# Optimization experiments

Hardware: AMD Instinct MI355X
Metric: run time of the kernel (lower is better)

Reference implementation:

```python
import jax, jax.numpy as jnp
import numpy as np

N_TYPES = 4
N_REL = 8
N_HEADS = 8
IN_DIM = 256
N_HID = 128
D_K = N_HID // N_HEADS
N_LAYERS = 2
N_NODES = 100000
N_EDGES = 400000


def setup_inputs() -> dict:
    key = jax.random.key(0)
    ks = jax.random.split(key, 24)
    s = 0.05
    inp = {
        'node_feature': jax.random.normal(ks[0], (N_NODES, IN_DIM), jnp.float32),
        'node_type': jax.random.randint(ks[1], (N_NODES,), 0, N_TYPES),
        'edge_index': jax.random.randint(ks[2], (2, N_EDGES), 0, N_NODES),
        'edge_type': jax.random.randint(ks[3], (N_EDGES,), 0, N_REL),
        # per-type input adapters
        'adapt_w': jax.random.normal(ks[4], (N_TYPES, IN_DIM, N_HID), jnp.float32) * s,
        'adapt_b': jnp.zeros((N_TYPES, N_HID), jnp.float32),
        # HGT conv params, stacked over layers
        'k_w': jax.random.normal(ks[5], (N_LAYERS, N_TYPES, N_HID, N_HID), jnp.float32) * s,
        'k_b': jnp.zeros((N_LAYERS, N_TYPES, N_HID), jnp.float32),
        'q_w': jax.random.normal(ks[6], (N_LAYERS, N_TYPES, N_HID, N_HID), jnp.float32) * s,
        'q_b': jnp.zeros((N_LAYERS, N_TYPES, N_HID), jnp.float32),
        'v_w': jax.random.normal(ks[7], (N_LAYERS, N_TYPES, N_HID, N_HID), jnp.float32) * s,
        'v_b': jnp.zeros((N_LAYERS, N_TYPES, N_HID), jnp.float32),
        'a_w': jax.random.normal(ks[8], (N_LAYERS, N_TYPES, N_HID, N_HID), jnp.float32) * s,
        'a_b': jnp.zeros((N_LAYERS, N_TYPES, N_HID), jnp.float32),
        'rel_pri': jnp.ones((N_LAYERS, N_REL, N_HEADS), jnp.float32),
        'rel_att': jnp.tile(jnp.eye(D_K, dtype=jnp.float32), (N_LAYERS, N_REL, N_HEADS, 1, 1))
                   + jax.random.normal(ks[9], (N_LAYERS, N_REL, N_HEADS, D_K, D_K), jnp.float32) * s,
        'rel_msg': jnp.tile(jnp.eye(D_K, dtype=jnp.float32), (N_LAYERS, N_REL, N_HEADS, 1, 1))
                   + jax.random.normal(ks[10], (N_LAYERS, N_REL, N_HEADS, D_K, D_K), jnp.float32) * s,
        'skip': jnp.ones((N_LAYERS, N_TYPES), jnp.float32),
    }
    return inp


def _per_type_linear(x, w, b, node_type, n_idx):
    # x: [N, din], w: [T, din, dout], b: [T, dout] -> gather row for each node's type
    h_all = jnp.einsum('ni,tio->tno', x, w) + b[:, None, :]  # [T, N, dout]
    return h_all[node_type, n_idx]  # [N, dout]


def _edge_softmax(score, tgt, n):
    # score: [E, H]; softmax over incoming edges of each target node
    m = jax.ops.segment_max(score, tgt, num_segments=n)  # [N, H]
    e = jnp.exp(score - m[tgt])
    z = jax.ops.segment_sum(e, tgt, num_segments=n)
    return e / (z[tgt] + 1e-9)


def _hgt_layer(x, node_type, src, tgt, edge_type,
               kw, kb, qw, qb, vw, vb, aw, ab, pri, att_m, msg_m, skip):
    n = x.shape[0]
    n_idx = jnp.arange(n)
    k = _per_type_linear(x, kw, kb, node_type, n_idx).reshape(n, N_HEADS, D_K)
    q = _per_type_linear(x, qw, qb, node_type, n_idx).reshape(n, N_HEADS, D_K)
    v = _per_type_linear(x, vw, vb, node_type, n_idx).reshape(n, N_HEADS, D_K)
    k_src, v_src, q_tgt = k[src], v[src], q[tgt]  # [E, H, dk]
    # per-relation attention/message transforms, accumulated over small fixed R
    k_rel = jnp.zeros_like(k_src)
    v_rel = jnp.zeros_like(v_src)
    for r in range(N_REL):
        msk = (edge_type == r)[:, None, None]
        k_rel = k_rel + jnp.einsum('ehd,hdf->ehf', jnp.where(msk, k_src, 0.0), att_m[r])
        v_rel = v_rel + jnp.einsum('ehd,hdf->ehf', jnp.where(msk, v_src, 0.0), msg_m[r])
    score = (q_tgt * k_rel).sum(-1) * pri[edge_type] * (1.0 / (D_K ** 0.5))  # [E, H]
    att = _edge_softmax(score, tgt, n)
    agg = jax.ops.segment_sum(att[..., None] * v_rel, tgt, num_segments=n)  # [N, H, dk]
    agg = agg.reshape(n, N_HID)
    trans = _per_type_linear(jax.nn.gelu(agg), aw, ab, node_type, n_idx)
    alpha = jax.nn.sigmoid(skip)[node_type][:, None]
    return trans * alpha + x * (1.0 - alpha)


def reference(node_feature, node_type, edge_index, edge_type,
              adapt_w, adapt_b, k_w, k_b, q_w, q_b, v_w, v_b,
              a_w, a_b, rel_pri, rel_att, rel_msg, skip):
    n = node_feature.shape[0]
    n_idx = jnp.arange(n)
    # per-node-type adapter + tanh (gather-linear-scatter, fully vectorized)
    h = jnp.tanh(_per_type_linear(node_feature, adapt_w, adapt_b, node_type, n_idx))
    src, tgt = edge_index[0], edge_index[1]
    for l in range(N_LAYERS):
        h = _hgt_layer(h, node_type, src, tgt, edge_type,
                       k_w[l], k_b[l], q_w[l], q_b[l], v_w[l], v_b[l],
                       a_w[l], a_b[l], rel_pri[l], rel_att[l], rel_msg[l], skip[l])
    return h
```

## Files before the change

### kernel.cpp

```cpp
#include <hip/hip_runtime.h>
#include <hip/hip_fp16.h>
#include <math.h>

constexpr int N_TYPES = 4;
constexpr int N_REL   = 8;
constexpr int N_HEADS = 8;
constexpr int IN_DIM  = 256;
constexpr int N_HID   = 128;
constexpr int D_K     = 16;
constexpr int N_LAYERS= 2;
constexpr int NN      = 100000;
constexpr int NE      = 400000;
constexpr int NBLK    = (NN + 255) / 256;

typedef _Float16 f16x8 __attribute__((ext_vector_type(8)));
typedef float    f32x4 __attribute__((ext_vector_type(4)));

__device__ __forceinline__ float gelu_f(float x) {
    const float c = 0.7978845608028654f;
    float x3 = x * x * x;
    return 0.5f * x * (1.0f + tanhf(c * (x + 0.044715f * x3)));
}
__device__ __forceinline__ float sigmoid_f(float x) {
    return 1.0f / (1.0f + expf(-x));
}

__global__ __launch_bounds__(256) void count2_kernel(
    const int* __restrict__ ntype, const int* __restrict__ tgt,
    unsigned* ncnt, unsigned* tcnt)
{
    int i = blockIdx.x * 256 + threadIdx.x;
    int lane = threadIdx.x & 63;
    int t = (i < NN) ? ntype[i] : -1;
    #pragma unroll
    for (int tt = 0; tt < N_TYPES; tt++) {
        unsigned long long m = __ballot(t == tt);
        if (m != 0ull && lane == __ffsll((unsigned long long)m) - 1)
            atomicAdd(&ncnt[tt], (unsigned)__popcll(m));
    }
    if (i < NE) atomicAdd(&tcnt[tgt[i]], 1u);
}

__global__ void node_offsets_kernel(unsigned* c)
{
    unsigned a = 0;
    for (int t = 0; t < N_TYPES; t++) { c[8 + t] = a; c[4 + t] = a; a += c[t]; }
    c[8 + N_TYPES] = a;
}

__global__ __launch_bounds__(256) void scan1_kernel(
    const unsigned* __restrict__ cnt, unsigned* __restrict__ eoff,
    unsigned* __restrict__ bsum)
{
    __shared__ unsigned sh[256];
    int i = blockIdx.x * 256 + threadIdx.x;
    unsigned v = (i < NN) ? cnt[i] : 0u;
    sh[threadIdx.x] = v;
    __syncthreads();
    for (int off = 1; off < 256; off <<= 1) {
        unsigned add = (threadIdx.x >= off) ? sh[threadIdx.x - off] : 0u;
        __syncthreads();
        sh[threadIdx.x] += add;
        __syncthreads();
    }
    if (i < NN) eoff[i] = sh[threadIdx.x] - v;
    if (threadIdx.x == 255) bsum[blockIdx.x] = sh[255];
}

__global__ __launch_bounds__(512) void scan2_kernel(unsigned* __restrict__ bsum)
{
    __shared__ unsigned sh[512];
    int i = threadIdx.x;
    unsigned v = (i < NBLK) ? bsum[i] : 0u;
    sh[i] = v;
    __syncthreads();
    for (int off = 1; off < 512; off <<= 1) {
        unsigned add = (i >= off) ? sh[i - off] : 0u;
        __syncthreads();
        sh[i] += add;
        __syncthreads();
    }
    if (i < NBLK) bsum[i] = sh[i] - v;
}

__global__ __launch_bounds__(256) void scan3_kernel(
    unsigned* __restrict__ eoff, const unsigned* __restrict__ bsum,
    unsigned* __restrict__ ecur)
{
    int i = blockIdx.x * 256 + threadIdx.x;
    if (i < NN) {
        unsigned v = eoff[i] + bsum[blockIdx.x];
        eoff[i] = v;
        ecur[i] = v;
    }
    if (i == 0) eoff[NN] = (unsigned)NE;
}

__global__ __launch_bounds__(256) void scatter2_kernel(
    const int* __restrict__ ntype,
    const int* __restrict__ src, const int* __restrict__ tgt,
    const int* __restrict__ etype,
    unsigned* ncur, unsigned* ecur,
    int* __restrict__ nidx,
    int* __restrict__ er_t)
{
    int i = blockIdx.x * 256 + threadIdx.x;
    int lane = threadIdx.x & 63;
    int t = (i < NN) ? ntype[i] : -1;
    #pragma unroll
    for (int tt = 0; tt < N_TYPES; tt++) {
        unsigned long long m = __ballot(t == tt);
        if (m == 0ull) continue;
        int leader = __ffsll((unsigned long long)m) - 1;
        unsigned base = 0;
        if (lane == leader) base = atomicAdd(&ncur[tt], (unsigned)__popcll(m));
        base = __shfl(base, leader, 64);
        if (t == tt) {
            unsigned rank = (unsigned)__popcll(m & ((1ull << lane) - 1ull));
            nidx[base + rank] = i;
        }
    }
    if (i < NE) {
        int tg = tgt[i];
        unsigned p = atomicAdd(&ecur[tg], 1u);
        er_t[p] = (src[i] << 3) | etype[i];
    }
}

__global__ __launch_bounds__(256) void cvt_wT_kernel(
    const float* __restrict__ W, __half* __restrict__ whT)
{
    int gid = blockIdx.x * 256 + threadIdx.x;
    constexpr int tot = 4 * 128 * 128;
    if (gid >= tot) return;
    int t = gid >> 14;
    int rem = gid & 16383;
    int k = rem >> 7, n = rem & 127;
    whT[(((size_t)t * 128 + n) << 7) + k] = __float2half(W[gid]);
}

template<int DIN, int OH>
__global__ __launch_bounds__(256) void ptl128_kernel(
    const float* __restrict__ x,
    const int* __restrict__ nidx,
    const unsigned* __restrict__ noff,
    const float* __restrict__ W,
    const float* __restrict__ Bb,
    void* __restrict__ out)
{
    constexpr int BK = 32;
    const int t = blockIdx.y;
    const unsigned s0 = noff[t], s1 = noff[t + 1];
    const unsigned base = s0 + blockIdx.x * 128u;
    if (base >= s1) return;
    const int nrows = (int)min(128u, s1 - base);

    __shared__ __align__(16) float xs[BK][128];
    __shared__ __align__(16) float wsl[BK][128];
    __shared__ int nid[128];

    const int tid = threadIdx.x;
    if (tid < 128) nid[tid] = nidx[base + (unsigned)min(tid, nrows - 1)];
    __syncthreads();

    const int tx = tid & 15;
    const int ty = tid >> 4;
    const int row = tid & 127, kg = tid >> 7;

    float acc[8][8];
    #pragma unroll
    for (int m = 0; m < 8; m++)
        #pragma unroll
        for (int j = 0; j < 8; j++) acc[m][j] = 0.0f;

    const float* Wt = W + (size_t)t * DIN * 128;

    for (int k0 = 0; k0 < DIN; k0 += BK) {
        {
            const float* xp = x + (size_t)nid[row] * DIN + k0 + kg * 16;
            float4 a0 = ((const float4*)xp)[0];
            float4 a1 = ((const float4*)xp)[1];
            float4 a2 = ((const float4*)xp)[2];
            float4 a3 = ((const float4*)xp)[3];
            float v[16] = {a0.x, a0.y, a0.z, a0.w, a1.x, a1.y, a1.z, a1.w,
                           a2.x, a2.y, a2.z, a2.w, a3.x, a3.y, a3.z, a3.w};
            #pragma unroll
            for (int i = 0; i < 16; i++) xs[kg * 16 + i][row] = v[i];
        }
        {
            const float* wp = Wt + (size_t)k0 * 128 + tid * 16;
            #pragma unroll
            for (int i = 0; i < 4; i++)
                *(float4*)&wsl[0][tid * 16 + 4 * i] = ((const float4*)wp)[i];
        }
        __syncthreads();
        #pragma unroll 8
        for (int kk = 0; kk < BK; kk++) {
            float4 xa = *(float4*)&xs[kk][ty * 8];
            float4 xb = *(float4*)&xs[kk][ty * 8 + 4];
            float4 wa = *(float4*)&wsl[kk][tx * 8];
            float4 wb = *(float4*)&wsl[kk][tx * 8 + 4];
            float xv[8] = {xa.x, xa.y, xa.z, xa.w, xb.x, xb.y, xb.z, xb.w};
            float wv[8] = {wa.x, wa.y, wa.z, wa.w, wb.x, wb.y, wb.z, wb.w};
            #pragma unroll
            for (int m = 0; m < 8; m++)
                #pragma unroll
                for (int j = 0; j < 8; j++)
                    acc[m][j] += xv[m] * wv[j];
        }
        __syncthreads();
    }

    float bb[8];
    #pragma unroll
    for (int j = 0; j < 8; j++) bb[j] = Bb[t * 128 + tx * 8 + j];

    #pragma unroll
    for (int m = 0; m < 8; m++) {
        int rr = ty * 8 + m;
        if (rr < nrows) {
            int n = nid[rr];
            float o[8];
            #pragma unroll
            for (int j = 0; j < 8; j++) o[j] = tanhf(acc[m][j] + bb[j]);
            if (OH == 0) {
                float* op = (float*)out + (size_t)n * 128 + tx * 8;
                *(float4*)(op)     = make_float4(o[0], o[1], o[2], o[3]);
                *(float4*)(op + 4) = make_float4(o[4], o[5], o[6], o[7]);
            } else {
                __align__(16) __half hh[8];
                #pragma unroll
                for (int j = 0; j < 8; j++) hh[j] = __float2half(o[j]);
                __half* op = (__half*)out + (size_t)n * 128 + tx * 8;
                *(uint4*)op = *(uint4*)hh;
            }
        }
    }
}

template<int MOUT, int OH>
__global__ __launch_bounds__(256) void mfma_ptl_kernel(
    const __half* __restrict__ xh,
    const int* __restrict__ nidx, const unsigned* __restrict__ noff,
    const __half* __restrict__ whT,
    const float* __restrict__ Bb,
    const float* __restrict__ skipv, const __half* __restrict__ hprev,
    void* __restrict__ out)
{
    constexpr int DIN = 128;
    const int t = blockIdx.y;
    const unsigned s0 = noff[t], s1 = noff[t + 1];
    const unsigned base = s0 + blockIdx.x * 128u;
    if (base >= s1) return;
    const int nrows = (int)min(128u, s1 - base);

    __shared__ __align__(16) ushort xsh[128][40];
    __shared__ __align__(16) ushort wsh[128][40];
    __shared__ int nid[128];

    const int tid = threadIdx.x;
    if (tid < 128) nid[tid] = nidx[base + (unsigned)min(tid, nrows - 1)];
    __syncthreads();

    const int lane = tid & 63;
    const int wave = tid >> 6;
    const int wr = wave >> 1, wc = wave & 1;
    const int lm = lane & 15, lk = lane >> 4;

    f32x4 acc[4][4];
    #pragma unroll
    for (int a = 0; a < 4; a++)
        #pragma unroll
        for (int b = 0; b < 4; b++)
            acc[a][b] = (f32x4){0.0f, 0.0f, 0.0f, 0.0f};

    const ushort* WT = (const ushort*)(whT + ((size_t)t << 14));
    const ushort* X  = (const ushort*)xh;

    const int srow = tid & 127, shalf = tid >> 7;
    const size_t xoff = (size_t)nid[srow] * DIN;

    for (int k0 = 0; k0 < DIN; k0 += 32) {
        {
            const ushort* ph = X + xoff + k0 + shalf * 16;
            *(uint4*)&xsh[srow][shalf * 16]     = *(const uint4*)ph;
            *(uint4*)&xsh[srow][shalf * 16 + 8] = *(const uint4*)(ph + 8);
            const ushort* qh = WT + ((size_t)srow << 7) + k0 + shalf * 16;
            *(uint4*)&wsh[srow][shalf * 16]     = *(const uint4*)qh;
            *(uint4*)&wsh[srow][shalf * 16 + 8] = *(const uint4*)(qh + 8);
        }
        __syncthreads();
        f16x8 ah[4];
        #pragma unroll
        for (int fm = 0; fm < 4; fm++)
            ah[fm] = *(const f16x8*)&xsh[wr * 64 + fm * 16 + lm][lk * 8];
        #pragma unroll
        for (int fn = 0; fn < 4; fn++) {
            f16x8 bh = *(const f16x8*)&wsh[wc * 64 + fn * 16 + lm][lk * 8];
            #pragma unroll
            for (int fm = 0; fm < 4; fm++)
                acc[fm][fn] = __builtin_amdgcn_mfma_f32_16x16x32_f16(
                    ah[fm], bh, acc[fm][fn], 0, 0, 0);
        }
        __syncthreads();
    }

    float alpha = 0.0f;
    if (MOUT == 2) alpha = sigmoid_f(skipv[t]);
    #pragma unroll
    for (int fn = 0; fn < 4; fn++) {
        const int dim = wc * 64 + fn * 16 + lm;
        const float bias = Bb[t * 128 + dim];
        #pragma unroll
        for (int fm = 0; fm < 4; fm++) {
            #pragma unroll
            for (int i = 0; i < 4; i++) {
                int rr = wr * 64 + fm * 16 + lk * 4 + i;
                if (rr < nrows) {
                    int n = nid[rr];
                    float o = acc[fm][fn][i] + bias;
                    if (MOUT == 2)
                        o = o * alpha +
                            __half2float(hprev[(size_t)n * 128 + dim]) * (1.0f - alpha);
                    if (OH == 0) ((float*)out)[(size_t)n * 128 + dim] = o;
                    else ((__half*)out)[(size_t)n * 128 + dim] = __float2half(o);
                }
            }
        }
    }
}

__global__ __launch_bounds__(256) void hgt_edge_fused(
    const int* __restrict__ er_t,
    const unsigned* __restrict__ eoff,
    const __half* __restrict__ kh,
    const __half* __restrict__ vh,
    const float* __restrict__ att,
    const float* __restrict__ msg,
    const float* __restrict__ pri,
    __half* __restrict__ qagg)
{
    __shared__ float aq_lds[2][1024];
    __shared__ float pv_lds[2][1024];
    const int tid  = threadIdx.x;
    const int tsel = tid >> 7;
    const int li   = tid & 127;
    const int h    = li >> 4;
    const int j    = li & 15;
    const int l    = tid & 63;
    const int hb   = tid & 0x30;
    const int t    = blockIdx.x * 2 + tsel;
    if (t >= NN) return;

    const unsigned e0 = eoff[t];
    const unsigned e1 = eoff[t + 1];
    const int deg = (int)(e1 - e0);

    if (deg == 0) {
        qagg[(size_t)t * 128 + li] = __float2half(0.0f);
        return;
    }

    float* al = aq_lds[tsel];
    float* pl = pv_lds[tsel];

    #pragma unroll
    for (int r = 0; r < 8; r++) pl[r * 128 + li] = 0.0f;

    const float qo = __half2float(qagg[(size_t)t * 128 + li]);
    float qh[16];
    #pragma unroll
    for (int f = 0; f < 16; f++) qh[f] = __shfl(qo, hb + f, 64);

    int pkl = 0;
    if (l < 16 && e0 + (unsigned)l < e1) pkl = er_t[e0 + l];

    const int dc = min(deg, 16);
    unsigned mask = 0;
    for (int c = 0; c < dc; ++c) mask |= 1u << (__shfl(pkl, c, 64) & 7);
    for (unsigned e = e0 + 16; e < e1; ++e) mask |= 1u << (er_t[e] & 7);

    unsigned need = mask;
    while (need) {
        const int r = __ffs(need) - 1; need &= need - 1;
        const float* Ar = att + (((r * 8 + h) * 16 + j) * 16);
        float4 A0 = ((const float4*)Ar)[0];
        float4 A1 = ((const float4*)Ar)[1];
        float4 A2 = ((const float4*)Ar)[2];
        float4 A3 = ((const float4*)Ar)[3];
        float acc =
            A0.x*qh[0]  + A0.y*qh[1]  + A0.z*qh[2]  + A0.w*qh[3]  +
            A1.x*qh[4]  + A1.y*qh[5]  + A1.z*qh[6]  + A1.w*qh[7]  +
            A2.x*qh[8]  + A2.y*qh[9]  + A2.z*qh[10] + A2.w*qh[11] +
            A3.x*qh[12] + A3.y*qh[13] + A3.z*qh[14] + A3.w*qh[15];
        al[r * 128 + li] = acc * pri[r * 8 + h] * 0.25f;
    }

    float z = 0.0f;
    float* plp = pl + li;
    const float* alp = al + li;
    const __half* kb = kh + li;
    const __half* vb = vh + li;

    unsigned e = e0;
    for (; e + 4 <= e1; e += 4) {
        const int o = (int)(e - e0);
        int p0, p1, p2, p3;
        if (o + 3 < 16) {
            p0 = __shfl(pkl, o + 0, 64);
            p1 = __shfl(pkl, o + 1, 64);
            p2 = __shfl(pkl, o + 2, 64);
            p3 = __shfl(pkl, o + 3, 64);
        } else {
            p0 = er_t[e + 0]; p1 = er_t[e + 1];
            p2 = er_t[e + 2]; p3 = er_t[e + 3];
        }
        const int o0 = (p0 & ~7) << 4;
        const int o1 = (p1 & ~7) << 4;
        const int o2 = (p2 & ~7) << 4;
        const int o3 = (p3 & ~7) << 4;
        const float k0 = __half2float(kb[o0]); const float v0 = __half2float(vb[o0]);
        const float k1 = __half2float(kb[o1]); const float v1 = __half2float(vb[o1]);
        const float k2 = __half2float(kb[o2]); const float v2 = __half2float(vb[o2]);
        const float k3 = __half2float(kb[o3]); const float v3 = __half2float(vb[o3]);
        float s0 = k0 * alp[(p0 & 7) * 128];
        float s1 = k1 * alp[(p1 & 7) * 128];
        float s2 = k2 * alp[(p2 & 7) * 128];
        float s3 = k3 * alp[(p3 & 7) * 128];
        s0 += __shfl_xor(s0, 1); s1 += __shfl_xor(s1, 1);
        s2 += __shfl_xor(s2, 1); s3 += __shfl_xor(s3, 1);
        s0 += __shfl_xor(s0, 2); s1 += __shfl_xor(s1, 2);
        s2 += __shfl_xor(s2, 2); s3 += __shfl_xor(s3, 2);
        s0 += __shfl_xor(s0, 4); s1 += __shfl_xor(s1, 4);
        s2 += __shfl_xor(s2, 4); s3 += __shfl_xor(s3, 4);
        s0 += __shfl_xor(s0, 8); s1 += __shfl_xor(s1, 8);
        s2 += __shfl_xor(s2, 8); s3 += __shfl_xor(s3, 8);
        const float q0 = __expf(s0 - 8.0f);
        const float q1 = __expf(s1 - 8.0f);
        const float q2 = __expf(s2 - 8.0f);
        const float q3 = __expf(s3 - 8.0f);
        z += q0 + q1 + q2 + q3;
        plp[(p0 & 7) * 128] += q0 * v0;
        plp[(p1 & 7) * 128] += q1 * v1;
        plp[(p2 & 7) * 128] += q2 * v2;
        plp[(p3 & 7) * 128] += q3 * v3;
    }
    if (e + 2 <= e1) {
        const int o = (int)(e - e0);
        int p0, p1;
        if (o + 1 < 16) { p0 = __shfl(pkl, o, 64); p1 = __shfl(pkl, o + 1, 64); }
        else            { p0 = er_t[e]; p1 = er_t[e + 1]; }
        const int o0 = (p0 & ~7) << 4;
        const int o1 = (p1 & ~7) << 4;
        const float k0 = __half2float(kb[o0]); const float v0 = __half2float(vb[o0]);
        const float k1 = __half2float(kb[o1]); const float v1 = __half2float(vb[o1]);
        float s0 = k0 * alp[(p0 & 7) * 128];
        float s1 = k1 * alp[(p1 & 7) * 128];
        s0 += __shfl_xor(s0, 1); s1 += __shfl_xor(s1, 1);
        s0 += __shfl_xor(s0, 2); s1 += __shfl_xor(s1, 2);
        s0 += __shfl_xor(s0, 4); s1 += __shfl_xor(s1, 4);
        s0 += __shfl_xor(s0, 8); s1 += __shfl_xor(s1, 8);
        const float q0 = __expf(s0 - 8.0f);
        const float q1 = __expf(s1 - 8.0f);
        z += q0 + q1;
        plp[(p0 & 7) * 128] += q0 * v0;
        plp[(p1 & 7) * 128] += q1 * v1;
        e += 2;
    }
    if (e < e1) {
        const int o = (int)(e - e0);
        const int p0 = (o < 16) ? __shfl(pkl, o, 64) : er_t[e];
        const int o0 = (p0 & ~7) << 4;
        const float k0 = __half2float(kb[o0]); const float v0 = __half2float(vb[o0]);
        float s0 = k0 * alp[(p0 & 7) * 128];
        s0 += __shfl_xor(s0, 1);
        s0 += __shfl_xor(s0, 2);
        s0 += __shfl_xor(s0, 4);
        s0 += __shfl_xor(s0, 8);
        const float q0 = __expf(s0 - 8.0f);
        z += q0;
        plp[(p0 & 7) * 128] += q0 * v0;
    }

    float acc = 0.0f;
    for (int r = 0; r < 8; r++) {
        if (!((mask >> r) & 1)) continue;
        const float* Mr = msg + ((r * 8 + h) * 256) + j;
        const float* sb = pl + r * 128 + h * 16;
        #pragma unroll
        for (int d = 0; d < 16; d++)
            acc += sb[d] * Mr[d * 16];
    }
    qagg[(size_t)t * 128 + li] =
        __float2half(gelu_f(acc * __frcp_rn(z + 1e-9f)));
}

extern "C" void kernel_launch(void* const* d_in, const int* in_sizes, int n_in,
                              void* d_out, int out_size, void* d_ws, size_t ws_size,
                              hipStream_t stream)
{
    const float* node_feature = (const float*)d_in[0];
    const int*   node_type    = (const int*)d_in[1];
    const int*   edge_index   = (const int*)d_in[2];
    const int*   edge_type    = (const int*)d_in[3];
    const float* adapt_w      = (const float*)d_in[4];
    const float* adapt_b      = (const float*)d_in[5];
    const float* k_w = (const float*)d_in[6];
    const float* k_b = (const float*)d_in[7];
    const float* q_w = (const float*)d_in[8];
    const float* q_b = (const float*)d_in[9];
    const float* v_w = (const float*)d_in[10];
    const float* v_b = (const float*)d_in[11];
    const float* a_w = (const float*)d_in[12];
    const float* a_b = (const float*)d_in[13];
    const float* rel_pri = (const float*)d_in[14];
    const float* rel_att = (const float*)d_in[15];
    const float* rel_msg = (const float*)d_in[16];
    const float* skip    = (const float*)d_in[17];

    const int* src = edge_index;
    const int* tgt = edge_index + NE;

    float* OUT = (float*)d_out;

    char* w = (char*)d_ws;
    auto alloc = [&](size_t bytes) -> void* {
        void* p = (void*)w;
        w += (bytes + 255) & ~(size_t)255;
        return p;
    };
    __half*   H0    = (__half*)alloc((size_t)NN * 128 * 2);
    __half*   H1    = (__half*)alloc((size_t)NN * 128 * 2);
    __half*   KH    = (__half*)alloc((size_t)NN * 128 * 2);
    __half*   VH    = (__half*)alloc((size_t)NN * 128 * 2);
    __half*   QA    = (__half*)alloc((size_t)NN * 128 * 2);
    __half*   WHT   = (__half*)alloc((size_t)8 * 4 * 128 * 128 * 2);
    int*      nidx  = (int*)alloc((size_t)NN * 4);
    int*      er_t  = (int*)alloc((size_t)NE * 4);
    unsigned* tcnt  = (unsigned*)alloc((size_t)NN * 4);
    unsigned* eoff  = (unsigned*)alloc((size_t)(NN + 1) * 4);
    unsigned* ecur  = (unsigned*)alloc((size_t)NN * 4);
    unsigned* bsum  = (unsigned*)alloc((size_t)NBLK * 4);
    unsigned* cnts  = (unsigned*)alloc(16 * 4);

    unsigned* ncnt = cnts;
    unsigned* ncur = cnts + 4;
    unsigned* noff = cnts + 8;

    hipMemsetAsync(cnts, 0, 16 * 4, stream);
    hipMemsetAsync(tcnt, 0, (size_t)NN * 4, stream);

    const int gblocks = (NE + 255) / 256;
    count2_kernel<<<gblocks, 256, 0, stream>>>(node_type, tgt, ncnt, tcnt);
    node_offsets_kernel<<<1, 1, 0, stream>>>(cnts);
    scan1_kernel<<<NBLK, 256, 0, stream>>>(tcnt, eoff, bsum);
    scan2_kernel<<<1, 512, 0, stream>>>(bsum);
    scan3_kernel<<<NBLK, 256, 0, stream>>>(eoff, bsum, ecur);
    scatter2_kernel<<<gblocks, 256, 0, stream>>>(node_type, src, tgt, edge_type,
                                                 ncur, ecur, nidx, er_t);

    {
        constexpr int wtot = 4 * 128 * 128;
        const int wblk = (wtot + 255) / 256;
        const float* Ws[8] = {
            k_w, q_w, v_w, a_w,
            k_w + (size_t)wtot, q_w + (size_t)wtot,
            v_w + (size_t)wtot, a_w + (size_t)wtot };
        for (int m = 0; m < 8; m++)
            cvt_wT_kernel<<<wblk, 256, 0, stream>>>(Ws[m], WHT + (size_t)m * wtot);
    }

    dim3 pgrid((NN + 127) / 128, N_TYPES);
    ptl128_kernel<IN_DIM, 1><<<pgrid, 256, 0, stream>>>(
        node_feature, nidx, noff, adapt_w, adapt_b, H0);

    const int fblocks = (NN + 1) / 2;
    const size_t wtot = (size_t)4 * 128 * 128;

    for (int l = 0; l < N_LAYERS; l++) {
        __half* hin = l ? H1 : H0;

        const __half* khT = WHT + (size_t)(l * 4 + 0) * wtot;
        const __half* qhT = WHT + (size_t)(l * 4 + 1) * wtot;
        const __half* vhT = WHT + (size_t)(l * 4 + 2) * wtot;
        const __half* ahT = WHT + (size_t)(l * 4 + 3) * wtot;

        const float* kbl = k_b + (size_t)l * N_TYPES * 128;
        const float* qbl = q_b + (size_t)l * N_TYPES * 128;
        const float* vbl = v_b + (size_t)l * N_TYPES * 128;
        const float* abl = a_b + (size_t)l * N_TYPES * 128;
        const float* pril = rel_pri + (size_t)l * N_REL * N_HEADS;
        const float* attl = rel_att + (size_t)l * N_REL * N_HEADS * D_K * D_K;
        const float* msgl = rel_msg + (size_t)l * N_REL * N_HEADS * D_K * D_K;
        const float* skipl = skip + (size_t)l * N_TYPES;

        mfma_ptl_kernel<1, 1><<<pgrid, 256, 0, stream>>>(
            hin, nidx, noff, khT, kbl, nullptr, nullptr, KH);
        mfma_ptl_kernel<1, 1><<<pgrid, 256, 0, stream>>>(
            hin, nidx, noff, qhT, qbl, nullptr, nullptr, QA);
        mfma_ptl_kernel<1, 1><<<pgrid, 256, 0, stream>>>(
            hin, nidx, noff, vhT, vbl, nullptr, nullptr, VH);

        hgt_edge_fused<<<fblocks, 256, 0, stream>>>(
            er_t, eoff, KH, VH, attl, msgl, pril, QA);

        if (l == 0)
            mfma_ptl_kernel<2, 1><<<pgrid, 256, 0, stream>>>(
                QA, nidx, noff, ahT, abl, skipl, hin, H1);
        else
            mfma_ptl_kernel<2, 0><<<pgrid, 256, 0, stream>>>(
                QA, nidx, noff, ahT, abl, skipl, hin, OUT);
    }
}
```

Baseline: 1.076 ms.

## Move adapter GEMM to MFMA and fuse K/Q/V projections into one kernel

Replaces the FP32 scalar-FMA input adapter GEMM with the fp16 MFMA per-type linear kernel. The kernel converts fp32 node features to half while staging them into shared memory, and adapter weights are pre-transposed to fp16. The three K/Q/V projection launches become one kernel that gathers each node row into shared memory once and reuses it for all three weight matrices. The eight per-matrix weight conversion launches collapse into a single launch. The half-precision adapter input may shift numerics slightly, and the fused kernel uses more shared memory per block.

```diff
diff --git a/kernel.cpp b/kernel.cpp
--- a/kernel.cpp
+++ b/kernel.cpp
@@ -127,165 +127,98 @@
     }
 }
 
-__global__ __launch_bounds__(256) void cvt_wT_kernel(
+__global__ __launch_bounds__(256) void cvt_w_layers_kernel(
+    const float* __restrict__ kw, const float* __restrict__ qw,
+    const float* __restrict__ vw, const float* __restrict__ aw,
+    __half* __restrict__ whT)
+{
+    int gid = blockIdx.x * 256 + threadIdx.x;
+    constexpr int per = 2 * 4 * 128 * 128;
+    if (gid >= 4 * per) return;
+    int m = gid >> 17;
+    int rem = gid & (per - 1);
+    const float* W = (m == 0) ? kw : (m == 1) ? qw : (m == 2) ? vw : aw;
+    float val = W[rem];
+    int l = rem >> 16;
+    int r2 = rem & 65535;
+    int t = r2 >> 14;
+    int r3 = r2 & 16383;
+    int k = r3 >> 7, n = r3 & 127;
+    whT[((size_t)(l * 4 + m) << 16) + ((size_t)t << 14) + (n << 7) + k] =
+        __float2half(val);
+}
+
+__global__ __launch_bounds__(256) void cvt_wA_kernel(
     const float* __restrict__ W, __half* __restrict__ whT)
 {
     int gid = blockIdx.x * 256 + threadIdx.x;
-    constexpr int tot = 4 * 128 * 128;
-    if (gid >= tot) return;
-    int t = gid >> 14;
-    int rem = gid & 16383;
+    if (gid >= 4 * 256 * 128) return;
+    int t = gid >> 15;
+    int rem = gid & 32767;
     int k = rem >> 7, n = rem & 127;
-    whT[(((size_t)t * 128 + n) << 7) + k] = __float2half(W[gid]);
-}
-
-template<int DIN, int OH>
-__global__ __launch_bounds__(256) void ptl128_kernel(
-    const float* __restrict__ x,
-    const int* __restrict__ nidx,
-    const unsigned* __restrict__ noff,
-    const float* __restrict__ W,
+    whT[((size_t)t * 128 + n) * 256 + k] = __float2half(W[gid]);
+}
+
+template<int DIN, int F32IN, int MOUT, int OH>
+__global__ __launch_bounds__(256) void mfma_ptl_kernel(
+    const void* __restrict__ x,
+    const int* __restrict__ nidx, const unsigned* __restrict__ noff,
+    const __half* __restrict__ whT,
     const float* __restrict__ Bb,
+    const float* __restrict__ skipv, const __half* __restrict__ hprev,
     void* __restrict__ out)
 {
-    constexpr int BK = 32;
     const int t = blockIdx.y;
     const unsigned s0 = noff[t], s1 = noff[t + 1];
     const unsigned base = s0 + blockIdx.x * 128u;
     if (base >= s1) return;
     const int nrows = (int)min(128u, s1 - base);
 
-    __shared__ __align__(16) float xs[BK][128];
-    __shared__ __align__(16) float wsl[BK][128];
+    __shared__ __align__(16) ushort xsh[128][40];
+    __shared__ __align__(16) ushort wsh[128][40];
     __shared__ int nid[128];
 
     const int tid = threadIdx.x;
     if (tid < 128) nid[tid] = nidx[base + (unsigned)min(tid, nrows - 1)];
     __syncthreads();
 
-    const int tx = tid & 15;
-    const int ty = tid >> 4;
-    const int row = tid & 127, kg = tid >> 7;
-
-    float acc[8][8];
+    const int lane = tid & 63;
+    const int wave = tid >> 6;
+    const int wr = wave >> 1, wc = wave & 1;
+    const int lm = lane & 15, lk = lane >> 4;
+
+    f32x4 acc[4][4];
     #pragma unroll
-    for (int m = 0; m < 8; m++)
-        #pragma unroll
-        for (int j = 0; j < 8; j++) acc[m][j] = 0.0f;
-
-    const float* Wt = W + (size_t)t * DIN * 128;
-
-    for (int k0 = 0; k0 < DIN; k0 += BK) {
-        {
-            const float* xp = x + (size_t)nid[row] * DIN + k0 + kg * 16;
+    for (int a = 0; a < 4; a++)
+        #pragma unroll
+        for (int b = 0; b < 4; b++)
+            acc[a][b] = (f32x4){0.0f, 0.0f, 0.0f, 0.0f};
+
+    const ushort* WT = (const ushort*)whT + (size_t)t * 128 * DIN;
+    const int srow = tid & 127, shalf = tid >> 7;
+    const size_t xoff = (size_t)nid[srow] * DIN;
+
+    for (int k0 = 0; k0 < DIN; k0 += 32) {
+        if (F32IN) {
+            const float* xp = (const float*)x + xoff + k0 + shalf * 16;
             float4 a0 = ((const float4*)xp)[0];
             float4 a1 = ((const float4*)xp)[1];
             float4 a2 = ((const float4*)xp)[2];
             float4 a3 = ((const float4*)xp)[3];
             float v[16] = {a0.x, a0.y, a0.z, a0.w, a1.x, a1.y, a1.z, a1.w,
                            a2.x, a2.y, a2.z, a2.w, a3.x, a3.y, a3.z, a3.w};
+            __align__(16) __half hh[16];
             #pragma unroll
-            for (int i = 0; i < 16; i++) xs[kg * 16 + i][row] = v[i];
-        }
-        {
-            const float* wp = Wt + (size_t)k0 * 128 + tid * 16;
-            #pragma unroll
-            for (int i = 0; i < 4; i++)
-                *(float4*)&wsl[0][tid * 16 + 4 * i] = ((const float4*)wp)[i];
-        }
-        __syncthreads();
-        #pragma unroll 8
-        for (int kk = 0; kk < BK; kk++) {
-            float4 xa = *(float4*)&xs[kk][ty * 8];
-            float4 xb = *(float4*)&xs[kk][ty * 8 + 4];
-            float4 wa = *(float4*)&wsl[kk][tx * 8];
-            float4 wb = *(float4*)&wsl[kk][tx * 8 + 4];
-            float xv[8] = {xa.x, xa.y, xa.z, xa.w, xb.x, xb.y, xb.z, xb.w};
-            float wv[8] = {wa.x, wa.y, wa.z, wa.w, wb.x, wb.y, wb.z, wb.w};
-            #pragma unroll
-            for (int m = 0; m < 8; m++)
-                #pragma unroll
-                for (int j = 0; j < 8; j++)
-                    acc[m][j] += xv[m] * wv[j];
-        }
-        __syncthreads();
-    }
-
-    float bb[8];
-    #pragma unroll
-    for (int j = 0; j < 8; j++) bb[j] = Bb[t * 128 + tx * 8 + j];
-
-    #pragma unroll
-    for (int m = 0; m < 8; m++) {
-        int rr = ty * 8 + m;
-        if (rr < nrows) {
-            int n = nid[rr];
-            float o[8];
-            #pragma unroll
-            for (int j = 0; j < 8; j++) o[j] = tanhf(acc[m][j] + bb[j]);
-            if (OH == 0) {
-                float* op = (float*)out + (size_t)n * 128 + tx * 8;
-                *(float4*)(op)     = make_float4(o[0], o[1], o[2], o[3]);
-                *(float4*)(op + 4) = make_float4(o[4], o[5], o[6], o[7]);
-            } else {
-                __align__(16) __half hh[8];
-                #pragma unroll
-                for (int j = 0; j < 8; j++) hh[j] = __float2half(o[j]);
-                __half* op = (__half*)out + (size_t)n * 128 + tx * 8;
-                *(uint4*)op = *(uint4*)hh;
-            }
-        }
-    }
-}
-
-template<int MOUT, int OH>
-__global__ __launch_bounds__(256) void mfma_ptl_kernel(
-    const __half* __restrict__ xh,
-    const int* __restrict__ nidx, const unsigned* __restrict__ noff,
-    const __half* __restrict__ whT,
-    const float* __restrict__ Bb,
-    const float* __restrict__ skipv, const __half* __restrict__ hprev,
-    void* __restrict__ out)
-{
-    constexpr int DIN = 128;
-    const int t = blockIdx.y;
-    const unsigned s0 = noff[t], s1 = noff[t + 1];
-    const unsigned base = s0 + blockIdx.x * 128u;
-    if (base >= s1) return;
-    const int nrows = (int)min(128u, s1 - base);
-
-    __shared__ __align__(16) ushort xsh[128][40];
-    __shared__ __align__(16) ushort wsh[128][40];
-    __shared__ int nid[128];
-
-    const int tid = threadIdx.x;
-    if (tid < 128) nid[tid] = nidx[base + (unsigned)min(tid, nrows - 1)];
-    __syncthreads();
-
-    const int lane = tid & 63;
-    const int wave = tid >> 6;
-    const int wr = wave >> 1, wc = wave & 1;
-    const int lm = lane & 15, lk = lane >> 4;
-
-    f32x4 acc[4][4];
-    #pragma unroll
-    for (int a = 0; a < 4; a++)
-        #pragma unroll
-        for (int b = 0; b < 4; b++)
-            acc[a][b] = (f32x4){0.0f, 0.0f, 0.0f, 0.0f};
-
-    const ushort* WT = (const ushort*)(whT + ((size_t)t << 14));
-    const ushort* X  = (const ushort*)xh;
-
-    const int srow = tid & 127, shalf = tid >> 7;
-    const size_t xoff = (size_t)nid[srow] * DIN;
-
-    for (int k0 = 0; k0 < DIN; k0 += 32) {
-        {
-            const ushort* ph = X + xoff + k0 + shalf * 16;
+            for (int i = 0; i < 16; i++) hh[i] = __float2half(v[i]);
+            *(uint4*)&xsh[srow][shalf * 16]     = ((uint4*)hh)[0];
+            *(uint4*)&xsh[srow][shalf * 16 + 8] = ((uint4*)hh)[1];
+        } else {
+            const ushort* ph = (const ushort*)x + xoff + k0 + shalf * 16;
             *(uint4*)&xsh[srow][shalf * 16]     = *(const uint4*)ph;
             *(uint4*)&xsh[srow][shalf * 16 + 8] = *(const uint4*)(ph + 8);
-            const ushort* qh = WT + ((size_t)srow << 7) + k0 + shalf * 16;
+        }
+        {
+            const ushort* qh = WT + (size_t)srow * DIN + k0 + shalf * 16;
             *(uint4*)&wsh[srow][shalf * 16]     = *(const uint4*)qh;
             *(uint4*)&wsh[srow][shalf * 16 + 8] = *(const uint4*)(qh + 8);
         }
@@ -319,11 +252,102 @@
                 if (rr < nrows) {
                     int n = nid[rr];
                     float o = acc[fm][fn][i] + bias;
-                    if (MOUT == 2)
+                    if (MOUT == 0) o = tanhf(o);
+                    else if (MOUT == 2)
                         o = o * alpha +
                             __half2float(hprev[(size_t)n * 128 + dim]) * (1.0f - alpha);
                     if (OH == 0) ((float*)out)[(size_t)n * 128 + dim] = o;
                     else ((__half*)out)[(size_t)n * 128 + dim] = __float2half(o);
+                }
+            }
+        }
+    }
+}
+
+__global__ __launch_bounds__(256) void mfma_kqv_kernel(
+    const __half* __restrict__ xh,
+    const int* __restrict__ nidx, const unsigned* __restrict__ noff,
+    const __half* __restrict__ wTk, const float* __restrict__ bk, __half* __restrict__ ok,
+    const __half* __restrict__ wTq, const float* __restrict__ bq, __half* __restrict__ oq,
+    const __half* __restrict__ wTv, const float* __restrict__ bv, __half* __restrict__ ov)
+{
+    const int t = blockIdx.y;
+    const unsigned s0 = noff[t], s1 = noff[t + 1];
+    const unsigned base = s0 + blockIdx.x * 128u;
+    if (base >= s1) return;
+    const int nrows = (int)min(128u, s1 - base);
+
+    __shared__ __align__(16) ushort xsh[128][136];
+    __shared__ __align__(16) ushort wsh[128][40];
+    __shared__ int nid[128];
+
+    const int tid = threadIdx.x;
+    if (tid < 128) nid[tid] = nidx[base + (unsigned)min(tid, nrows - 1)];
+    __syncthreads();
+
+    const int srow = tid & 127, shalf = tid >> 7;
+    {
+        const ushort* xp = (const ushort*)xh + (size_t)nid[srow] * 128 + shalf * 64;
+        #pragma unroll
+        for (int i = 0; i < 8; i++)
+            *(uint4*)&xsh[srow][shalf * 64 + i * 8] = ((const uint4*)xp)[i];
+    }
+
+    const int lane = tid & 63;
+    const int wave = tid >> 6;
+    const int wr = wave >> 1, wc = wave & 1;
+    const int lm = lane & 15, lk = lane >> 4;
+
+    const ushort* WTs[3] = { (const ushort*)wTk + ((size_t)t << 14),
+                             (const ushort*)wTq + ((size_t)t << 14),
+                             (const ushort*)wTv + ((size_t)t << 14) };
+    const float* Bs[3] = { bk, bq, bv };
+    __half* Os[3] = { ok, oq, ov };
+
+    #pragma unroll
+    for (int w = 0; w < 3; w++) {
+        f32x4 acc[4][4];
+        #pragma unroll
+        for (int a = 0; a < 4; a++)
+            #pragma unroll
+            for (int b = 0; b < 4; b++)
+                acc[a][b] = (f32x4){0.0f, 0.0f, 0.0f, 0.0f};
+
+        for (int k0 = 0; k0 < 128; k0 += 32) {
+            __syncthreads();
+            {
+                const ushort* qh = WTs[w] + ((size_t)srow << 7) + k0 + shalf * 16;
+                *(uint4*)&wsh[srow][shalf * 16]     = *(const uint4*)qh;
+                *(uint4*)&wsh[srow][shalf * 16 + 8] = *(const uint4*)(qh + 8);
+            }
+            __syncthreads();
+            f16x8 ah[4];
+            #pragma unroll
+            for (int fm = 0; fm < 4; fm++)
+                ah[fm] = *(const f16x8*)&xsh[wr * 64 + fm * 16 + lm][k0 + lk * 8];
+            #pragma unroll
+            for (int fn = 0; fn < 4; fn++) {
+                f16x8 bh = *(const f16x8*)&wsh[wc * 64 + fn * 16 + lm][lk * 8];
+                #pragma unroll
+                for (int fm = 0; fm < 4; fm++)
+                    acc[fm][fn] = __builtin_amdgcn_mfma_f32_16x16x32_f16(
+                        ah[fm], bh, acc[fm][fn], 0, 0, 0);
+            }
+        }
+        #pragma unroll
+        for (int fn = 0; fn < 4; fn++) {
+            const int dim = wc * 64 + fn * 16 + lm;
+            const float bias = Bs[w][t * 128 + dim];
+            #pragma unroll
+            for (int fm = 0; fm < 4; fm++) {
+                #pragma unroll
+                for (int i = 0; i < 4; i++) {
+                    int rr = wr * 64 + fm * 16 + lk * 4 + i;
+                    if (rr < nrows) {
+                        int n = nid[rr];
+                        Os[w][(size_t)n * 128 + dim] =
+                            __float2half(acc[fm][fn][i] + bias);
+                    }
                 }
             }
         }
@@ -535,6 +559,7 @@
     __half*   VH    = (__half*)alloc((size_t)NN * 128 * 2);
     __half*   QA    = (__half*)alloc((size_t)NN * 128 * 2);
     __half*   WHT   = (__half*)alloc((size_t)8 * 4 * 128 * 128 * 2);
+    __half*   WAT   = (__half*)alloc((size_t)4 * 128 * 256 * 2);
     int*      nidx  = (int*)alloc((size_t)NN * 4);
     int*      er_t  = (int*)alloc((size_t)NE * 4);
     unsigned* tcnt  = (unsigned*)alloc((size_t)NN * 4);
@@ -559,20 +584,13 @@
     scatter2_kernel<<<gblocks, 256, 0, stream>>>(node_type, src, tgt, edge_type,
                                                  ncur, ecur, nidx, er_t);
 
-    {
-        constexpr int wtot = 4 * 128 * 128;
-        const int wblk = (wtot + 255) / 256;
-        const float* Ws[8] = {
-            k_w, q_w, v_w, a_w,
-            k_w + (size_t)wtot, q_w + (size_t)wtot,
-            v_w + (size_t)wtot, a_w + (size_t)wtot };
-        for (int m = 0; m < 8; m++)
-            cvt_wT_kernel<<<wblk, 256, 0, stream>>>(Ws[m], WHT + (size_t)m * wtot);
-    }
+    cvt_w_layers_kernel<<<(4 * 2 * 4 * 128 * 128 + 255) / 256, 256, 0, stream>>>(
+        k_w, q_w, v_w, a_w, WHT);
+    cvt_wA_kernel<<<(4 * 256 * 128 + 255) / 256, 256, 0, stream>>>(adapt_w, WAT);
 
     dim3 pgrid((NN + 127) / 128, N_TYPES);
-    ptl128_kernel<IN_DIM, 1><<<pgrid, 256, 0, stream>>>(
-        node_feature, nidx, noff, adapt_w, adapt_b, H0);
+    mfma_ptl_kernel<IN_DIM, 1, 0, 1><<<pgrid, 256, 0, stream>>>(
+        node_feature, nidx, noff, WAT, adapt_b, nullptr, nullptr, H0);
 
     const int fblocks = (NN + 1) / 2;
     const size_t wtot = (size_t)4 * 128 * 128;
@@ -594,21 +612,20 @@
         const float* msgl = rel_msg + (size_t)l * N_REL * N_HEADS * D_K * D_K;
         const float* skipl = skip + (size_t)l * N_TYPES;
 
-        mfma_ptl_kernel<1, 1><<<pgrid, 256, 0, stream>>>(
-            hin, nidx, noff, khT, kbl, nullptr, nullptr, KH);
-        mfma_ptl_kernel<1, 1><<<pgrid, 256, 0, stream>>>(
-            hin, nidx, noff, qhT, qbl, nullptr, nullptr, QA);
-        mfma_ptl_kernel<1, 1><<<pgrid, 256, 0, stream>>>(
-            hin, nidx, noff, vhT, vbl, nullptr, nullptr, VH);
+        mfma_kqv_kernel<<<pgrid, 256, 0, stream>>>(
+            hin, nidx, noff,
+            khT, kbl, KH,
+            qhT, qbl, QA,
+            vhT, vbl, VH);
 
         hgt_edge_fused<<<fblocks, 256, 0, stream>>>(
             er_t, eoff, KH, VH, attl, msgl, pril, QA);
 
         if (l == 0)
-            mfma_ptl_kernel<2, 1><<<pgrid, 256, 0, stream>>>(
-                QA, nidx, noff, ahT, abl, skipl, hin, H1);
+            mfma_ptl_kernel<N_HID, 0, 2, 1><<<pgrid, 256, 0, stream>>>(
+                QA, nidx, noff, ahT, abl, skipl, H0, H1);
         else
-            mfma_ptl_kernel<2, 0><<<pgrid, 256, 0, stream>>>(
-                QA, nidx, noff, ahT, abl, skipl, hin, OUT);
-    }
-}
+            mfma_ptl_kernel<N_HID, 0, 2, 0><<<pgrid, 256, 0, stream>>>(
+                QA, nidx, noff, ahT, abl, skipl, H1, OUT);
+    }
+}
```

Result: faster. 1.024 ms (-4.8%).
